# Kernel optimization log

Measured on AMD Instinct MI355X. Metric: run time of the kernel, lower is better.

## Reference

```python
import jax, jax.numpy as jnp
import numpy as np

B, N, DIM = 2, 1024, 512
HEADS, DIM_HEAD = 8, 64
HIDDEN = HEADS * DIM_HEAD
TIME_DIM = 512
BIAS_DIM = 16
EPS = 1e-5


def setup_inputs() -> dict:
    key = jax.random.key(0)
    ks = jax.random.split(key, 12)
    inp = {
        "x": jax.random.normal(ks[0], (B, N, DIM), jnp.float32),
        "residx": jnp.broadcast_to(jnp.arange(N, dtype=jnp.float32), (B, N)),
        "time": jax.random.normal(ks[1], (B, 1, TIME_DIM), jnp.float32),
        "attn_bias": jax.random.normal(ks[2], (B, BIAS_DIM, N, N), jnp.float32),
        "seq_mask": jnp.ones((B, N), jnp.float32),
        # params
        "gamma": jnp.ones((DIM,), jnp.float32),
        "Wt": jax.random.normal(ks[3], (2 * DIM, TIME_DIM), jnp.float32) * 0.02,
        "bt": jax.random.normal(ks[4], (2 * DIM,), jnp.float32) * 0.02,
        "Wb": jax.random.normal(ks[5], (HEADS, BIAS_DIM), jnp.float32) * 0.1,
        "bb": jax.random.normal(ks[6], (HEADS,), jnp.float32) * 0.1,
        "Wq": jax.random.normal(ks[7], (HIDDEN, DIM), jnp.float32) * (DIM ** -0.5),
        "Wkv": jax.random.normal(ks[8], (2 * HIDDEN, DIM), jnp.float32) * (DIM ** -0.5),
        "Wo": jax.random.normal(ks[9], (DIM, HIDDEN), jnp.float32) * (HIDDEN ** -0.5),
    }
    return inp


def _layer_norm(x, gamma):
    mu = jnp.mean(x, axis=-1, keepdims=True)
    var = jnp.var(x, axis=-1, keepdims=True)
    return (x - mu) * jax.lax.rsqrt(var + EPS) * gamma  # beta buffer is zeros


def reference(x, residx, time, attn_bias, seq_mask, gamma, Wt, bt, Wb, bb, Wq, Wkv, Wo):
    h, d = HEADS, DIM_HEAD
    b, n, _ = x.shape
    xn = _layer_norm(x, gamma)
    # time conditioning: SiLU -> Linear -> chunk into scale/shift
    t = jax.nn.silu(time) @ Wt.T + bt  # [B,1,2*dim]
    scale, shift = jnp.split(t, 2, axis=-1)
    xn = xn * (scale + 1.0) + shift
    xn = xn * seq_mask[..., None]
    # projections
    q = (xn @ Wq.T).reshape(b, n, h, d).transpose(0, 2, 1, 3)  # b h n d
    kv = xn @ Wkv.T
    k_, v_ = jnp.split(kv, 2, axis=-1)
    k = k_.reshape(b, n, h, d).transpose(0, 2, 1, 3)
    v = v_.reshape(b, n, h, d).transpose(0, 2, 1, 3)
    q = q * (d ** -0.5)
    sim = jnp.einsum('bhid,bhjd->bhij', q, k)
    # attn bias projection: b a i j -> linear over a -> b h i j
    bias = jnp.einsum('baij,ha->bhij', attn_bias, Wb) + bb[None, :, None, None]
    sim = sim + bias
    # mask
    attn_mask = seq_mask[:, None, :, None] * seq_mask[:, None, None, :]  # b 1 i j
    sim = sim - (1.0 - attn_mask) * 1e6
    attn = jax.nn.softmax(sim, axis=-1)
    out = jnp.einsum('bhij,bhjd->bhid', attn, v)
    out = out.transpose(0, 2, 1, 3).reshape(b, n, h * d)
    out = out @ Wo.T
    out = out * seq_mask[..., None]
    return out
```

## Files before the change

kernel.cpp:

```cpp
#include <hip/hip_runtime.h>
#include <cstdint>
#include <cstddef>

typedef __bf16 bf16x8 __attribute__((ext_vector_type(8)));
typedef float f32x4 __attribute__((ext_vector_type(4)));
typedef unsigned short u16;
typedef unsigned short u16x8 __attribute__((ext_vector_type(8)));

__device__ __forceinline__ u16 f2b(float f) {
    union { float f; uint32_t u; } v; v.f = f;
    uint32_t r = v.u + 0x7fffu + ((v.u >> 16) & 1u);
    return (u16)(r >> 16);
}
__device__ __forceinline__ float b2f(u16 h) {
    union { uint32_t u; float f; } v; v.u = ((uint32_t)h) << 16; return v.f;
}

__global__ __launch_bounds__(256) void prep_kernel(
    const float* __restrict__ Wq, const float* __restrict__ Wkv, const float* __restrict__ Wo,
    const float* __restrict__ timep, const float* __restrict__ Wt, const float* __restrict__ bt,
    u16* __restrict__ wqkv, u16* __restrict__ wo, float* __restrict__ tbuf)
{
    __shared__ float st[512];
    int bx = blockIdx.x, tid = threadIdx.x;
    if (bx < 1024) {
        int i = bx * 256 + tid;
        float4 v; u16* dp;
        if (i < 65536)      { v = ((const float4*)Wq)[i];            dp = wqkv + (size_t)i * 4; }
        else if (i < 196608){ int k = i - 65536;  v = ((const float4*)Wkv)[k]; dp = wqkv + 262144 + (size_t)k * 4; }
        else                { int k = i - 196608; v = ((const float4*)Wo)[k];  dp = wo + (size_t)k * 4; }
        ushort4 o;
        o.x = f2b(v.x); o.y = f2b(v.y); o.z = f2b(v.z); o.w = f2b(v.w);
        *(ushort4*)dp = o;
    } else {
        int bx2 = bx - 1024;
        int b = bx2 >> 2, ch = bx2 & 3;
        for (int k = tid; k < 512; k += 256) {
            float v = timep[b * 512 + k];
            st[k] = v / (1.f + __expf(-v));
        }
        __syncthreads();
        int o = ch * 256 + tid;
        const float4* wrow = (const float4*)(Wt + (size_t)o * 512);
        float acc = bt[o];
        #pragma unroll 4
        for (int k4 = 0; k4 < 128; k4++) {
            float4 w = wrow[k4];
            acc += st[k4*4+0]*w.x + st[k4*4+1]*w.y + st[k4*4+2]*w.z + st[k4*4+3]*w.w;
        }
        tbuf[b * 1024 + o] = acc;
    }
}

__global__ __launch_bounds__(64) void ln_cond_kernel(
    const float* __restrict__ x, const float* __restrict__ gamma,
    const float* __restrict__ tbuf, const float* __restrict__ seq_mask,
    u16* __restrict__ xn)
{
    int m = blockIdx.x;
    int b = m >> 10;
    int lane = threadIdx.x;
    const float* xr = x + (size_t)m * 512;
    int c0 = lane * 8;
    float4 v0 = *(const float4*)(xr + c0);
    float4 v1 = *(const float4*)(xr + c0 + 4);
    float xv[8] = {v0.x, v0.y, v0.z, v0.w, v1.x, v1.y, v1.z, v1.w};
    float s = 0.f, ss = 0.f;
    #pragma unroll
    for (int e = 0; e < 8; e++) { s += xv[e]; ss += xv[e]*xv[e]; }
    #pragma unroll
    for (int off = 1; off < 64; off <<= 1) {
        s  += __shfl_xor(s, off);
        ss += __shfl_xor(ss, off);
    }
    float mu = s * (1.f/512.f);
    float var = ss * (1.f/512.f) - mu*mu;
    float rs = rsqrtf(var + 1e-5f);
    float mk = seq_mask[m];
    u16x8 ov;
    #pragma unroll
    for (int e = 0; e < 8; e++) {
        int c = c0 + e;
        float sc = tbuf[b*1024 + c] + 1.f;
        float sh = tbuf[b*1024 + 512 + c];
        float val = ((xv[e] - mu) * rs * gamma[c] * sc + sh) * mk;
        ov[e] = f2b(val);
    }
    *(u16x8*)&xn[(size_t)m * 512 + c0] = ov;
}

__global__ __launch_bounds__(256) void qkv_bias_kernel(
    const float* __restrict__ ab, const float* __restrict__ Wb, const float* __restrict__ bbv,
    const u16* __restrict__ xn, const u16* __restrict__ wqkv,
    u16* __restrict__ bias_t, u16* __restrict__ qb, u16* __restrict__ kb, u16* __restrict__ vT)
{
    __shared__ u16 As[128][40];
    __shared__ u16 Bs[128][40];
    __shared__ float wbs[128];
    __shared__ float bbs[8];
    const int tid = threadIdx.x;
    const int bx = blockIdx.x;
    if (bx < 2048) {
        if (tid < 128) wbs[tid] = Wb[tid];
        if (tid < 8) bbs[tid] = bbv[tid];
        __syncthreads();
        int t = bx * 256 + tid;
        int b = t >> 18;
        int rem = t & 262143;
        int r  = rem & 3;
        int li = (rem >> 2) & 15;
        int jt = (rem >> 6) & 15;
        int i4 = rem >> 10;
        int i  = i4*4 + r;
        int it32 = i4 >> 3, isub = (i4 >> 2) & 1, g = i4 & 3;
        int slot = isub*64 + g*16 + li;
        int voff = (i << 10) + jt*64 + li;

        float acc[8][4] = {};
        #pragma unroll
        for (int a8 = 0; a8 < 2; a8++) {
            float v[8][4];
            #pragma unroll
            for (int aa = 0; aa < 8; aa++) {
                const float* pp = ab + (((size_t)(b*16 + a8*8 + aa)) << 20) + voff;
                #pragma unroll
                for (int fj = 0; fj < 4; fj++) v[aa][fj] = pp[fj*16];
            }
            #pragma unroll
            for (int aa = 0; aa < 8; aa++)
                #pragma unroll
                for (int h = 0; h < 8; h++) {
                    float w = wbs[h*16 + a8*8 + aa];
                    #pragma unroll
                    for (int fj = 0; fj < 4; fj++) acc[h][fj] += w * v[aa][fj];
                }
        }
        #pragma unroll
        for (int h = 0; h < 8; h++) {
            float bv = bbs[h];
            ushort4 o;
            o.x = f2b(acc[h][0] + bv); o.y = f2b(acc[h][1] + bv);
            o.z = f2b(acc[h][2] + bv); o.w = f2b(acc[h][3] + bv);
            size_t addr = ((((size_t)(b*8 + h))*32 + it32)*16 + jt)*2048 + slot*16 + r*4;
            *(ushort4*)&bias_t[addr] = o;
        }
    } else {
        int v = bx - 2048;
        const int m0 = (v & 15) * 128, n0 = (v >> 4) * 128;
        const int lane = tid & 63, wid = tid >> 6;
        const int wr = wid >> 1, wc = wid & 1;
        const int li = lane & 15, g = lane >> 4;
        f32x4 acc[4][4] = {};
        const int srow = tid >> 2, scol = (tid & 3) * 8;
        for (int k0 = 0; k0 < 512; k0 += 32) {
            *(bf16x8*)&As[srow][scol]      = *(const bf16x8*)&xn[(size_t)(m0+srow)*512 + k0 + scol];
            *(bf16x8*)&As[srow+64][scol]   = *(const bf16x8*)&xn[(size_t)(m0+srow+64)*512 + k0 + scol];
            *(bf16x8*)&Bs[srow][scol]      = *(const bf16x8*)&wqkv[(size_t)(n0+srow)*512 + k0 + scol];
            *(bf16x8*)&Bs[srow+64][scol]   = *(const bf16x8*)&wqkv[(size_t)(n0+srow+64)*512 + k0 + scol];
            __syncthreads();
            bf16x8 a[4], bf[4];
            #pragma unroll
            for (int mi = 0; mi < 4; mi++) a[mi]  = *(const bf16x8*)&As[wr*64 + mi*16 + li][g*8];
            #pragma unroll
            for (int nj = 0; nj < 4; nj++) bf[nj] = *(const bf16x8*)&Bs[wc*64 + nj*16 + li][g*8];
            #pragma unroll
            for (int mi = 0; mi < 4; mi++)
                #pragma unroll
                for (int nj = 0; nj < 4; nj++)
                    acc[mi][nj] = __builtin_amdgcn_mfma_f32_16x16x32_bf16(a[mi], bf[nj], acc[mi][nj], 0, 0, 0);
            __syncthreads();
        }
        #pragma unroll
        for (int mi = 0; mi < 4; mi++)
            #pragma unroll
            for (int nj = 0; nj < 4; nj++) {
                int o = n0 + wc*64 + nj*16 + li;
                int m_base = m0 + wr*64 + mi*16 + g*4;
                if (o < 1024) {
                    #pragma unroll
                    for (int r = 0; r < 4; r++) {
                        int m = m_base + r;
                        int b = m >> 10, n = m & 1023;
                        float vv = acc[mi][nj][r];
                        if (o < 512) {
                            qb[((size_t)(b*8 + (o>>6))*1024 + n)*64 + (o&63)] = f2b(vv * 0.125f);
                        } else {
                            int oo = o - 512;
                            kb[((size_t)(b*8 + (oo>>6))*1024 + n)*64 + (oo&63)] = f2b(vv);
                        }
                    }
                } else {
                    int oo = o - 1024;
                    int b = m_base >> 10, n = m_base & 1023;
                    ushort4 ov;
                    ov.x = f2b(acc[mi][nj][0]); ov.y = f2b(acc[mi][nj][1]);
                    ov.z = f2b(acc[mi][nj][2]); ov.w = f2b(acc[mi][nj][3]);
                    *(ushort4*)&vT[((size_t)(b*8 + (oo>>6))*64 + (oo&63))*1024 + n] = ov;
                }
            }
    }
}

__global__ __launch_bounds__(256) void attn_kernel(
    const u16* __restrict__ qb, const u16* __restrict__ kb, const u16* __restrict__ vT,
    const u16* __restrict__ bias_t, const float* __restrict__ seq_mask,
    float* __restrict__ Om, float* __restrict__ ml)
{
    __shared__ u16 Ks[2][4096];
    __shared__ u16 Vs[2][4096];
    __shared__ u16 Ps[4][1024];
    __shared__ float mjs[512];
    int tid = threadIdx.x;
    int lane = tid & 63, w = tid >> 6;
    int li = lane & 15, g = lane >> 4;
    int it = blockIdx.x, h = blockIdx.y;
    int bz = blockIdx.z;
    int b = bz >> 1, jh = bz & 1;
    int bh = b*8 + h;
    int i0 = it * 64;
    int jt0 = jh * 8;
    const u16* qp = qb + ((size_t)bh*1024 + i0) * 64;
    const u16* kp = kb + (size_t)bh*65536 + (size_t)jt0*4096;
    const u16* vp = vT + (size_t)bh*65536;
    const u16* bp = bias_t + (((size_t)(bh*32 + it*2 + (w>>1)))*16 + jt0)*2048 + ((w&1)*64 + lane)*16;

    if (tid < 128) ((float4*)mjs)[tid] = ((const float4*)(seq_mask + b*1024 + jh*512))[tid];

    bf16x8 aq0 = *(const bf16x8*)&qp[(w*16 + li)*64 + g*8];
    bf16x8 aq1 = *(const bf16x8*)&qp[(w*16 + li)*64 + 32 + g*8];

    const int sli = tid & 15, sg = (tid >> 4) & 3, sf = tid >> 6;
    const int kslot0 = (sf*128 + sg*16 + sli) * 8;
    bf16x8 kr0, kr1, vr0, vr1, bfA_c, bfB_c, bfA_n, bfB_n;
    #define LOADT(jx) do { \
        kr0 = *(const bf16x8*)&kp[(size_t)(jx)*4096 + (sf*16 + sli)*64 + sg*8]; \
        kr1 = *(const bf16x8*)&kp[(size_t)(jx)*4096 + (sf*16 + sli)*64 + 32 + sg*8]; \
        vr0 = *(const bf16x8*)&vp[(size_t)(sf*16 + sli)*1024 + (jt0+(jx))*64 + sg*8]; \
        vr1 = *(const bf16x8*)&vp[(size_t)(sf*16 + sli)*1024 + (jt0+(jx))*64 + 32 + sg*8]; \
        bfA_n = *(const bf16x8*)&bp[(size_t)(jx)*2048]; \
        bfB_n = *(const bf16x8*)&bp[(size_t)(jx)*2048 + 8]; \
    } while (0)
    #define STORET(buf_) do { \
        *(bf16x8*)&Ks[buf_][kslot0]       = kr0; \
        *(bf16x8*)&Ks[buf_][kslot0 + 512] = kr1; \
        *(bf16x8*)&Vs[buf_][kslot0]       = vr0; \
        *(bf16x8*)&Vs[buf_][kslot0 + 512] = vr1; \
    } while (0)

    f32x4 oacc[4] = {};
    float m_run[4], l_run[4], mi[4];
    #pragma unroll
    for (int r = 0; r < 4; r++) {
        m_run[r] = -3e38f; l_run[r] = 0.f;
        mi[r] = seq_mask[b*1024 + i0 + w*16 + g*4 + r];
    }

    LOADT(0); STORET(0); bfA_c = bfA_n; bfB_c = bfB_n;
    __syncthreads();

    for (int jtt = 0; jtt < 8; jtt++) {
        int cur = jtt & 1;
        if (jtt < 7) LOADT(jtt + 1);
        f32x4 s[4] = {};
        #pragma unroll
        for (int fj = 0; fj < 4; fj++) {
            bf16x8 bk0 = *(const bf16x8*)&Ks[cur][(fj*128 + g*16 + li)*8];
            bf16x8 bk1 = *(const bf16x8*)&Ks[cur][(fj*128 + g*16 + li)*8 + 512];
            s[fj] = __builtin_amdgcn_mfma_f32_16x16x32_bf16(aq0, bk0, s[fj], 0, 0, 0);
            s[fj] = __builtin_amdgcn_mfma_f32_16x16x32_bf16(aq1, bk1, s[fj], 0, 0, 0);
        }
        float pmax[4] = {-3e38f, -3e38f, -3e38f, -3e38f};
        #pragma unroll
        for (int fj = 0; fj < 4; fj++) {
            float mj = mjs[jtt*64 + fj*16 + li];
            #pragma unroll
            for (int r = 0; r < 4; r++) {
                float bvl = (r < 2) ? b2f(((u16x8)bfA_c)[r*4 + fj]) : b2f(((u16x8)bfB_c)[(r-2)*4 + fj]);
                float sv = s[fj][r] + bvl;
                sv -= (1.f - mi[r]*mj) * 1e6f;
                s[fj][r] = sv;
                pmax[r] = fmaxf(pmax[r], sv);
            }
        }
        #pragma unroll
        for (int r = 0; r < 4; r++)
            #pragma unroll
            for (int off = 1; off < 16; off <<= 1)
                pmax[r] = fmaxf(pmax[r], __shfl_xor(pmax[r], off));
        float alpha[4], psum[4] = {0.f, 0.f, 0.f, 0.f}, mnew[4];
        #pragma unroll
        for (int r = 0; r < 4; r++) {
            mnew[r] = fmaxf(m_run[r], pmax[r]);
            alpha[r] = __expf(m_run[r] - mnew[r]);
            m_run[r] = mnew[r];
        }
        #pragma unroll
        for (int fj = 0; fj < 4; fj++)
            #pragma unroll
            for (int r = 0; r < 4; r++) {
                float p = __expf(s[fj][r] - mnew[r]);
                s[fj][r] = p;
                psum[r] += p;
            }
        #pragma unroll
        for (int r = 0; r < 4; r++) {
            #pragma unroll
            for (int off = 1; off < 16; off <<= 1) psum[r] += __shfl_xor(psum[r], off);
            l_run[r] = l_run[r]*alpha[r] + psum[r];
        }
        #pragma unroll
        for (int fj = 0; fj < 4; fj++) {
            int ph2 = fj >> 1;
            int pg = (fj*2 + (li >> 3)) & 3;
            int pin = li & 7;
            #pragma unroll
            for (int r = 0; r < 4; r++)
                Ps[w][(ph2*64 + pg*16 + g*4 + r)*8 + pin] = f2b(s[fj][r]);
        }
        #pragma unroll
        for (int fd = 0; fd < 4; fd++)
            #pragma unroll
            for (int r = 0; r < 4; r++)
                oacc[fd][r] *= alpha[r];
        bf16x8 ap0 = *(const bf16x8*)&Ps[w][(g*16 + li)*8];
        bf16x8 ap1 = *(const bf16x8*)&Ps[w][(g*16 + li)*8 + 512];
        #pragma unroll
        for (int fd = 0; fd < 4; fd++) {
            bf16x8 bv0 = *(const bf16x8*)&Vs[cur][(fd*128 + g*16 + li)*8];
            bf16x8 bv1 = *(const bf16x8*)&Vs[cur][(fd*128 + g*16 + li)*8 + 512];
            oacc[fd] = __builtin_amdgcn_mfma_f32_16x16x32_bf16(ap0, bv0, oacc[fd], 0, 0, 0);
            oacc[fd] = __builtin_amdgcn_mfma_f32_16x16x32_bf16(ap1, bv1, oacc[fd], 0, 0, 0);
        }
        if (jtt < 7) { STORET(cur ^ 1); bfA_c = bfA_n; bfB_c = bfB_n; }
        __syncthreads();
    }
    size_t pbase = ((size_t)(bh*16 + it)*2 + jh) * 4096;
    #pragma unroll
    for (int fd = 0; fd < 4; fd++)
        #pragma unroll
        for (int r = 0; r < 4; r++)
            Om[pbase + (size_t)(w*16 + g*4 + r)*64 + fd*16 + li] = oacc[fd][r];
    if (li == 0) {
        #pragma unroll
        for (int r = 0; r < 4; r++) {
            size_t mb = ((size_t)(bh*16 + it)*2 + jh) * 128 + (w*16 + g*4 + r)*2;
            ml[mb] = m_run[r]; ml[mb + 1] = l_run[r];
        }
    }
    #undef LOADT
    #undef STORET
}

__global__ __launch_bounds__(256) void merge_kernel(
    const float* __restrict__ Om, const float* __restrict__ ml, u16* __restrict__ aout)
{
    int blk = blockIdx.x;
    int bh = blk >> 4, it = blk & 15;
    int b = bh >> 3, h = bh & 7;
    int tid = threadIdx.x;
    int row = tid >> 2, dc = (tid & 3) * 16;
    size_t p0 = ((size_t)blk*2 + 0)*4096 + (size_t)row*64 + dc;
    size_t p1 = ((size_t)blk*2 + 1)*4096 + (size_t)row*64 + dc;
    size_t m0i = ((size_t)blk*2 + 0)*128 + row*2;
    size_t m1i = ((size_t)blk*2 + 1)*128 + row*2;
    float m0 = ml[m0i], l0 = ml[m0i + 1];
    float m1 = ml[m1i], l1 = ml[m1i + 1];
    float mm = fmaxf(m0, m1);
    float e0 = __expf(m0 - mm), e1 = __expf(m1 - mm);
    float linv = 1.f / (l0*e0 + l1*e1);
    int i = it*64 + row;
    u16* op = &aout[((size_t)(b*1024 + i))*512 + h*64 + dc];
    #pragma unroll
    for (int c4 = 0; c4 < 4; c4++) {
        f32x4 v0 = *(const f32x4*)&Om[p0 + c4*4];
        f32x4 v1 = *(const f32x4*)&Om[p1 + c4*4];
        ushort4 o;
        o.x = f2b((v0[0]*e0 + v1[0]*e1)*linv);
        o.y = f2b((v0[1]*e0 + v1[1]*e1)*linv);
        o.z = f2b((v0[2]*e0 + v1[2]*e1)*linv);
        o.w = f2b((v0[3]*e0 + v1[3]*e1)*linv);
        *(ushort4*)&op[c4*4] = o;
    }
}

__global__ __launch_bounds__(256) void out_gemm_kernel(
    const u16* __restrict__ aout, const u16* __restrict__ wo,
    const float* __restrict__ seq_mask, float* __restrict__ out)
{
    __shared__ u16 As[64][40];
    __shared__ u16 Bs[64][40];
    const int tid = threadIdx.x;
    const int lane = tid & 63, wid = tid >> 6;
    const int wr = wid >> 1, wc = wid & 1;
    const int li = lane & 15, g = lane >> 4;
    const int m0 = blockIdx.x * 64, n0 = blockIdx.y * 64;

    f32x4 acc[2][2] = {};
    const int lrow = tid >> 2, lcol = (tid & 3) * 8;
    for (int k0 = 0; k0 < 512; k0 += 32) {
        *(bf16x8*)&As[lrow][lcol] = *(const bf16x8*)&aout[(size_t)(m0+lrow)*512 + k0 + lcol];
        *(bf16x8*)&Bs[lrow][lcol] = *(const bf16x8*)&wo[(size_t)(n0+lrow)*512 + k0 + lcol];
        __syncthreads();
        bf16x8 a[2], bf[2];
        #pragma unroll
        for (int fi = 0; fi < 2; fi++) a[fi]  = *(const bf16x8*)&As[wr*32 + fi*16 + li][g*8];
        #pragma unroll
        for (int fj = 0; fj < 2; fj++) bf[fj] = *(const bf16x8*)&Bs[wc*32 + fj*16 + li][g*8];
        #pragma unroll
        for (int fi = 0; fi < 2; fi++)
            #pragma unroll
            for (int fj = 0; fj < 2; fj++)
                acc[fi][fj] = __builtin_amdgcn_mfma_f32_16x16x32_bf16(a[fi], bf[fj], acc[fi][fj], 0, 0, 0);
        __syncthreads();
    }
    #pragma unroll
    for (int fi = 0; fi < 2; fi++)
        #pragma unroll
        for (int fj = 0; fj < 2; fj++)
            #pragma unroll
            for (int r = 0; r < 4; r++) {
                int m = m0 + wr*32 + fi*16 + g*4 + r;
                int o = n0 + wc*32 + fj*16 + li;
                out[(size_t)m*512 + o] = acc[fi][fj][r] * seq_mask[m];
            }
}

extern "C" void kernel_launch(void* const* d_in, const int* in_sizes, int n_in,
                              void* d_out, int out_size, void* d_ws, size_t ws_size,
                              hipStream_t stream) {
    const float* x         = (const float*)d_in[0];
    const float* timep     = (const float*)d_in[2];
    const float* attn_bias = (const float*)d_in[3];
    const float* seq_mask  = (const float*)d_in[4];
    const float* gamma     = (const float*)d_in[5];
    const float* Wt        = (const float*)d_in[6];
    const float* bt        = (const float*)d_in[7];
    const float* Wb        = (const float*)d_in[8];
    const float* bb        = (const float*)d_in[9];
    const float* Wq        = (const float*)d_in[10];
    const float* Wkv       = (const float*)d_in[11];
    const float* Wo        = (const float*)d_in[12];
    float* out = (float*)d_out;

    char* ws = (char*)d_ws;
    size_t off = 0;
    auto alloc = [&](size_t bytes) { char* p = ws + off; off += (bytes + 255) & ~(size_t)255; return p; };
    float* tbuf  = (float*)alloc(2 * 1024 * 4);
    u16* xn      = (u16*)alloc((size_t)2048 * 512 * 2);
    u16* wqkv    = (u16*)alloc((size_t)1536 * 512 * 2);
    u16* wo      = (u16*)alloc((size_t)512 * 512 * 2);
    u16* qb      = (u16*)alloc((size_t)2 * 8 * 1024 * 64 * 2);
    u16* kb      = (u16*)alloc((size_t)2 * 8 * 1024 * 64 * 2);
    u16* vT      = (u16*)alloc((size_t)2 * 8 * 64 * 1024 * 2);
    u16* bias_t  = (u16*)alloc((size_t)2 * 8 * 1024 * 1024 * 2);
    u16* aout    = (u16*)alloc((size_t)2048 * 512 * 2);
    float* Om    = (float*)alloc((size_t)256 * 2 * 4096 * 4);
    float* ml    = (float*)alloc((size_t)256 * 2 * 128 * 4);
    (void)ws_size;

    prep_kernel<<<1032, 256, 0, stream>>>(Wq, Wkv, Wo, timep, Wt, bt, wqkv, wo, tbuf);
    ln_cond_kernel<<<2048, 64, 0, stream>>>(x, gamma, tbuf, seq_mask, xn);
    qkv_bias_kernel<<<2240, 256, 0, stream>>>(attn_bias, Wb, bb, xn, wqkv, bias_t, qb, kb, vT);
    attn_kernel<<<dim3(16, 8, 4), 256, 0, stream>>>(qb, kb, vT, bias_t, seq_mask, Om, ml);
    merge_kernel<<<256, 256, 0, stream>>>(Om, ml, aout);
    out_gemm_kernel<<<dim3(32, 8), 256, 0, stream>>>(aout, wo, seq_mask, out);
}
```

Before: 95.58 us.

## Vectorize attn_bias projection loads and transpose output through shared memory

```diff
diff --git a/kernel.cpp b/kernel.cpp
--- a/kernel.cpp
+++ b/kernel.cpp
@@ -89,6 +89,7 @@
     *(u16x8*)&xn[(size_t)m * 512 + c0] = ov;
 }
 
+#define TST 68
 __global__ __launch_bounds__(256) void qkv_bias_kernel(
     const float* __restrict__ ab, const float* __restrict__ Wb, const float* __restrict__ bbv,
     const u16* __restrict__ xn, const u16* __restrict__ wqkv,
@@ -96,56 +97,65 @@
 {
     __shared__ u16 As[128][40];
     __shared__ u16 Bs[128][40];
+    __shared__ u16 Ts[8 * 16 * TST];
     __shared__ float wbs[128];
     __shared__ float bbs[8];
     const int tid = threadIdx.x;
     const int bx = blockIdx.x;
-    if (bx < 2048) {
+    if (bx >= 192) {
         if (tid < 128) wbs[tid] = Wb[tid];
         if (tid < 8) bbs[tid] = bbv[tid];
         __syncthreads();
-        int t = bx * 256 + tid;
-        int b = t >> 18;
-        int rem = t & 262143;
-        int r  = rem & 3;
-        int li = (rem >> 2) & 15;
-        int jt = (rem >> 6) & 15;
-        int i4 = rem >> 10;
-        int i  = i4*4 + r;
-        int it32 = i4 >> 3, isub = (i4 >> 2) & 1, g = i4 & 3;
-        int slot = isub*64 + g*16 + li;
-        int voff = (i << 10) + jt*64 + li;
-
-        float acc[8][4] = {};
-        #pragma unroll
-        for (int a8 = 0; a8 < 2; a8++) {
-            float v[8][4];
-            #pragma unroll
-            for (int aa = 0; aa < 8; aa++) {
-                const float* pp = ab + (((size_t)(b*16 + a8*8 + aa)) << 20) + voff;
-                #pragma unroll
-                for (int fj = 0; fj < 4; fj++) v[aa][fj] = pp[fj*16];
-            }
-            #pragma unroll
-            for (int aa = 0; aa < 8; aa++)
-                #pragma unroll
-                for (int h = 0; h < 8; h++) {
-                    float w = wbs[h*16 + a8*8 + aa];
-                    #pragma unroll
-                    for (int fj = 0; fj < 4; fj++) acc[h][fj] += w * v[aa][fj];
-                }
-        }
+        int bx2 = bx - 192;
+        int b = bx2 >> 10;
+        int rem = bx2 & 1023;
+        int i16 = rem >> 4;
+        int jt  = rem & 15;
+        int il = tid >> 4, jq = tid & 15;
+        int i = i16*16 + il;
+        int j = jt*64 + jq*4;
+        const float* base = ab + (((size_t)b << 24)) + ((size_t)i << 10) + j;
+
+        f32x4 v[16];
+        #pragma unroll
+        for (int a = 0; a < 16; a++)
+            v[a] = *(const f32x4*)(base + ((size_t)a << 20));
+        f32x4 acc[8];
         #pragma unroll
         for (int h = 0; h < 8; h++) {
             float bv = bbs[h];
+            acc[h][0] = bv; acc[h][1] = bv; acc[h][2] = bv; acc[h][3] = bv;
+        }
+        #pragma unroll
+        for (int a = 0; a < 16; a++)
+            #pragma unroll
+            for (int h = 0; h < 8; h++)
+                acc[h] += wbs[h*16 + a] * v[a];
+        #pragma unroll
+        for (int h = 0; h < 8; h++) {
             ushort4 o;
-            o.x = f2b(acc[h][0] + bv); o.y = f2b(acc[h][1] + bv);
-            o.z = f2b(acc[h][2] + bv); o.w = f2b(acc[h][3] + bv);
-            size_t addr = ((((size_t)(b*8 + h))*32 + it32)*16 + jt)*2048 + slot*16 + r*4;
-            *(ushort4*)&bias_t[addr] = o;
+            o.x = f2b(acc[h][0]); o.y = f2b(acc[h][1]); o.z = f2b(acc[h][2]); o.w = f2b(acc[h][3]);
+            *(ushort4*)&Ts[(h*16 + il)*TST + jq*4] = o;
+        }
+        __syncthreads();
+        int hh = tid >> 5;
+        int s0 = tid & 31;
+        size_t tilebase = ((((size_t)(b*8 + hh))*32 + (i16 >> 1))*16 + jt)*2048 + (size_t)(i16 & 1)*1024;
+        #pragma unroll
+        for (int ss = 0; ss < 2; ss++) {
+            int slot = s0 + ss*32;
+            int g = slot >> 4, li = slot & 15;
+            u16 tmp[16];
+            #pragma unroll
+            for (int r = 0; r < 4; r++)
+                #pragma unroll
+                for (int fj = 0; fj < 4; fj++)
+                    tmp[r*4 + fj] = Ts[(hh*16 + g*4 + r)*TST + fj*16 + li];
+            *(uint4*)&bias_t[tilebase + (size_t)slot*16]     = *(uint4*)&tmp[0];
+            *(uint4*)&bias_t[tilebase + (size_t)slot*16 + 8] = *(uint4*)&tmp[8];
         }
     } else {
-        int v = bx - 2048;
+        int v = bx;
         const int m0 = (v & 15) * 128, n0 = (v >> 4) * 128;
         const int lane = tid & 63, wid = tid >> 6;
         const int wr = wid >> 1, wc = wid & 1;
```

New measurement: 88.10 us. 7.8% less time.
